# Kernel tuning notes

Measured on AMD Instinct MI355X. Metric: run time of the kernel, lower is better.

## Reference

```python
import jax, jax.numpy as jnp
import numpy as np

NN = 262144        # total nodes = 4096 graphs * 64 nodes
EN = 524288        # directed edges
IN_DIM = 32
H = 128
PROP_STEPS = 3


def setup_inputs() -> dict:
    key = jax.random.key(0)
    ks = jax.random.split(key, 16)
    s = lambda d: 1.0 / np.sqrt(d)
    x = jax.random.normal(ks[0], (NN, IN_DIM), dtype=jnp.float32)
    # edges: random within each 64-node graph block would be most faithful; random
    # over NN is the same access pattern workload-wise. Use per-graph-local edges.
    src = jax.random.randint(ks[1], (EN,), 0, NN, dtype=jnp.int64)
    dst = jax.random.randint(ks[2], (EN,), 0, NN, dtype=jnp.int64)
    edge_index = jnp.stack([src, dst], axis=0)
    return {
        "x": x,
        "edge_index": edge_index,
        "W_in": jax.random.normal(ks[3], (IN_DIM, H), jnp.float32) * s(IN_DIM),
        "b_in": jnp.zeros((H,), jnp.float32),
        "W_e1": jax.random.normal(ks[4], (H, H), jnp.float32) * s(H),
        "b_e1": jnp.zeros((H,), jnp.float32),
        "W_e2": jax.random.normal(ks[5], (H, H), jnp.float32) * s(H),
        "b_e2": jnp.zeros((H,), jnp.float32),
        "W_ih": jax.random.normal(ks[6], (H, 3 * H), jnp.float32) * s(H),
        "b_ih": jnp.zeros((3 * H,), jnp.float32),
        "W_hh": jax.random.normal(ks[7], (H, 3 * H), jnp.float32) * s(H),
        "b_hh": jnp.zeros((3 * H,), jnp.float32),
        "W_out": jax.random.normal(ks[8], (H, 1), jnp.float32) * s(H),
        "b_out": jnp.zeros((1,), jnp.float32),
    }


def reference(x, edge_index, W_in, b_in, W_e1, b_e1, W_e2, b_e2,
              W_ih, b_ih, W_hh, b_hh, W_out, b_out):
    in_node, out_node = edge_index[0], edge_index[1]
    nn = x.shape[0]
    # input MLP: Linear + tanh
    h = jnp.tanh(x @ W_in + b_in)                         # [NN, H]
    for _ in range(PROP_STEPS):
        # unified edge MLP (hidden tanh + linear out), applied per node then gathered
        m = jnp.tanh(h @ W_e1 + b_e1) @ W_e2 + b_e2       # [NN, H]
        msg = m[in_node]                                  # [EN, H] gather
        ssum = jax.ops.segment_sum(msg, out_node, num_segments=nn)
        cnt = jax.ops.segment_sum(jnp.ones((msg.shape[0],), msg.dtype),
                                  out_node, num_segments=nn)
        m_agg = ssum / jnp.maximum(cnt, 1.0)[:, None]     # scatter_mean, [NN, H]
        # GRU cell update: input = m_agg, hidden = h (torch GRUCell math)
        gi = m_agg @ W_ih + b_ih                          # [NN, 3H]
        gh = h @ W_hh + b_hh                              # [NN, 3H]
        i_r, i_z, i_n = jnp.split(gi, 3, axis=-1)
        h_r, h_z, h_n = jnp.split(gh, 3, axis=-1)
        r = jax.nn.sigmoid(i_r + h_r)
        z = jax.nn.sigmoid(i_z + h_z)
        n = jnp.tanh(i_n + r * h_n)
        h = (1.0 - z) * n + z * h
    # unified output head: single Linear
    return h @ W_out + b_out                              # [NN, 1]
```

## Files before the change

kernel.cpp:

```cpp
#include <hip/hip_runtime.h>

#define NN 262144
#define EN 524288
#define HD 128
#define IND 32

#define NT64  (NN/64)
#define GRID_E 768
#define GRID_G 1024

typedef __attribute__((ext_vector_type(8))) short s16x8;
typedef __attribute__((ext_vector_type(4))) float f32x4;
typedef unsigned short u16;
typedef unsigned int u32;

#define MFMA(a,b,c) __builtin_amdgcn_mfma_f32_16x16x32_bf16(a,b,c,0,0,0)
#define SWZ(p) ((p) ^ ((((p)>>8)&7)<<4))

typedef __attribute__((address_space(1))) void gas_void;
typedef __attribute__((address_space(3))) void las_void;
__device__ __forceinline__ void gload16(const void* g, void* l){
  __builtin_amdgcn_global_load_lds((gas_void*)g, (las_void*)l, 16, 0, 0);
}

__device__ __forceinline__ u16 f2b(float f){
  u32 u = __builtin_bit_cast(u32, f);
  u = (u + 0x7fffu + ((u >> 16) & 1u)) >> 16;
  return (u16)u;
}
__device__ __forceinline__ u32 cvtpk(float lo, float hi){
  return (u32)f2b(lo) | ((u32)f2b(hi) << 16);
}
__device__ __forceinline__ float b2f(u32 lo16){ return __builtin_bit_cast(float, lo16 << 16); }
__device__ __forceinline__ float rcpf_(float x){ return __builtin_amdgcn_rcpf(x); }
__device__ __forceinline__ float exp2_(float x){ return __builtin_amdgcn_exp2f(x); }
__device__ __forceinline__ float fsig(float x){ return rcpf_(1.f + exp2_(x * -1.442695041f)); }
__device__ __forceinline__ float ftanh(float x){ return fmaf(-2.f, rcpf_(1.f + exp2_(x * 2.885390082f)), 1.f); }

__global__ __launch_bounds__(256) void k_w2bt(const float* __restrict__ W, u16* __restrict__ Wt, int K, int N){
  int idx = blockIdx.x*256 + threadIdx.x;
  if (idx >= K*N) return;
  int n = idx / K, k = idx - n*K;
  Wt[idx] = f2b(W[k*N + n]);
}

__global__ void k_eflag(const int* __restrict__ ei, int* __restrict__ flag){
  int v = ei[threadIdx.x*2 + 1];
  unsigned long long b = __ballot(v != 0);
  if (threadIdx.x == 0) flag[0] = (b == 0ULL) ? 1 : 0;
}
__device__ __forceinline__ int eget(const int* ei, int f, int which, int e){
  return f ? ei[(which*EN + e)*2] : ei[which*EN + e];
}

__global__ __launch_bounds__(256) void k_count(const int* __restrict__ ei, const int* __restrict__ flag, int* __restrict__ cnt){
  int e = blockIdx.x*256 + threadIdx.x;
  if (e < EN) atomicAdd(&cnt[eget(ei, flag[0], 1, e)], 1);
}
__global__ __launch_bounds__(256) void k_scan1(const int* __restrict__ cnt, int* __restrict__ excl, int* __restrict__ bsum){
  __shared__ int ws[4];
  int i = blockIdx.x*256 + threadIdx.x;
  int v = cnt[i];
  int ln = threadIdx.x & 63;
  int x = v;
  #pragma unroll
  for (int d=1; d<64; d<<=1){ int y = __shfl_up(x, d); if (ln >= d) x += y; }
  if (ln == 63) ws[threadIdx.x>>6] = x;
  __syncthreads();
  int wpre = 0;
  for (int j=0; j<(threadIdx.x>>6); ++j) wpre += ws[j];
  excl[i] = wpre + x - v;
  if (threadIdx.x == 255) bsum[blockIdx.x] = wpre + x;
}
__global__ __launch_bounds__(1024) void k_scan2(int* __restrict__ bsum){
  __shared__ int ws[16];
  int i = threadIdx.x;
  int v = bsum[i];
  int ln = i & 63;
  int x = v;
  #pragma unroll
  for (int d=1; d<64; d<<=1){ int y = __shfl_up(x, d); if (ln >= d) x += y; }
  if (ln == 63) ws[i>>6] = x;
  __syncthreads();
  int wpre = 0;
  for (int j=0; j<(i>>6); ++j) wpre += ws[j];
  bsum[i] = wpre + x - v;
}
__global__ __launch_bounds__(256) void k_scan3(const int* __restrict__ excl, const int* __restrict__ bsum, int* __restrict__ rp, int* __restrict__ cur){
  int i = blockIdx.x*256 + threadIdx.x;
  int v = excl[i] + bsum[blockIdx.x];
  rp[i] = v; cur[i] = v;
  if (i == 0) rp[NN] = EN;
}
__global__ __launch_bounds__(256) void k_fill(const int* __restrict__ ei, const int* __restrict__ flag, int* __restrict__ cur, int* __restrict__ cx){
  int e = blockIdx.x*256 + threadIdx.x;
  if (e >= EN) return;
  int f = flag[0];
  int p = atomicAdd(&cur[eget(ei, f, 1, e)], 1);
  cx[p] = eget(ei, f, 0, e);
}

__global__ __launch_bounds__(256) void k_input(const float* __restrict__ x, const u16* __restrict__ wt, const float* __restrict__ bias, u16* __restrict__ h){
  const int wv = threadIdx.x >> 6, ln = threadIdx.x & 63;
  const int l15 = ln & 15, lg = ln >> 4;
  const int base = blockIdx.x*128 + wv*32;
  s16x8 a[2];
  #pragma unroll
  for (int rt=0; rt<2; ++rt){
    const float* xp = x + (base + rt*16 + l15)*IND + lg*8;
    float4 v0 = *reinterpret_cast<const float4*>(xp);
    float4 v1 = *reinterpret_cast<const float4*>(xp + 4);
    s16x8 t;
    t[0]=(short)f2b(v0.x); t[1]=(short)f2b(v0.y); t[2]=(short)f2b(v0.z); t[3]=(short)f2b(v0.w);
    t[4]=(short)f2b(v1.x); t[5]=(short)f2b(v1.y); t[6]=(short)f2b(v1.z); t[7]=(short)f2b(v1.w);
    a[rt] = t;
  }
  #pragma unroll
  for (int cg=0; cg<8; ++cg){
    const int col = cg*16 + l15;
    s16x8 bf = *reinterpret_cast<const s16x8*>(wt + col*IND + lg*8);
    float bb = bias[col];
    f32x4 acc0 = {bb,bb,bb,bb}, acc1 = {bb,bb,bb,bb};
    acc0 = MFMA(a[0], bf, acc0);
    acc1 = MFMA(a[1], bf, acc1);
    #pragma unroll
    for (int r=0; r<4; ++r){
      h[(size_t)(base + lg*4 + r)*HD + col]      = f2b(ftanh(acc0[r]));
      h[(size_t)(base + 16 + lg*4 + r)*HD + col] = f2b(ftanh(acc1[r]));
    }
  }
}

__global__ __launch_bounds__(512) void k_edge(const u16* __restrict__ h, const u16* __restrict__ wt1, const float* __restrict__ b1,
                                              const u16* __restrict__ wt2, const float* __restrict__ b2, u16* __restrict__ m){
  extern __shared__ __align__(1024) unsigned char lds[];
  const int tid = threadIdx.x, wv = tid >> 6, ln = tid & 63;
  const int l15 = ln & 15, lg = ln >> 4;
  const int col = wv*16 + l15;

  s16x8 B1[4], B2[4];
  #pragma unroll
  for (int kk=0; kk<4; ++kk){
    const int ko = kk*32 + lg*8;
    B1[kk] = *reinterpret_cast<const s16x8*>(wt1 + (size_t)col*HD + ko);
    B2[kk] = *reinterpret_cast<const s16x8*>(wt2 + (size_t)col*HD + ko);
  }
  const float b1s = b1[col], b2s = b2[col];

  {
    const unsigned char* hg = (const unsigned char*)h + (size_t)blockIdx.x*64*256;
    #pragma unroll
    for (int i=0; i<2; ++i){
      int c = wv*2 + i;
      int p = c*1024 + ln*16;
      gload16(hg + SWZ(p), lds + c*1024);
    }
  }
  __syncthreads();

  unsigned char* tl = lds + 32768;
  int t = 0;
  #pragma unroll 1
  for (int tt = blockIdx.x; tt < NT64; tt += GRID_E, ++t){
    if (tt + GRID_E < NT64){
      const unsigned char* hg = (const unsigned char*)h + (size_t)(tt+GRID_E)*64*256;
      unsigned char* dst = lds + ((t+1)&1)*16384;
      #pragma unroll
      for (int i=0; i<2; ++i){
        int c = wv*2 + i;
        int p = c*1024 + ln*16;
        gload16(hg + SWZ(p), dst + c*1024);
      }
    }
    const unsigned char* hl = lds + (t&1)*16384;
    for (int rt=0; rt<4; ++rt){
      s16x8 a[4];
      #pragma unroll
      for (int kk=0; kk<4; ++kk){
        int row = rt*16 + l15;
        int p = row*256 + (((kk*4+lg) ^ (row&7))<<4);
        a[kk] = *reinterpret_cast<const s16x8*>(hl + p);
      }
      f32x4 acc = {b1s,b1s,b1s,b1s};
      __builtin_amdgcn_s_setprio(1);
      #pragma unroll
      for (int kk=0; kk<4; ++kk) acc = MFMA(a[kk], B1[kk], acc);
      __builtin_amdgcn_s_setprio(0);
      #pragma unroll
      for (int r=0; r<4; ++r){
        int row = rt*16 + lg*4 + r;
        int tb = row*256 + ((((col*2)>>4) ^ (row&7))<<4) + ((col&7)*2);
        *reinterpret_cast<u16*>(tl + tb) = f2b(ftanh(acc[r]));
      }
    }
    __syncthreads();
    for (int rt=0; rt<4; ++rt){
      s16x8 a[4];
      #pragma unroll
      for (int kk=0; kk<4; ++kk){
        int row = rt*16 + l15;
        int p = row*256 + (((kk*4+lg) ^ (row&7))<<4);
        a[kk] = *reinterpret_cast<const s16x8*>(tl + p);
      }
      f32x4 acc = {b2s,b2s,b2s,b2s};
      __builtin_amdgcn_s_setprio(1);
      #pragma unroll
      for (int kk=0; kk<4; ++kk) acc = MFMA(a[kk], B2[kk], acc);
      __builtin_amdgcn_s_setprio(0);
      u16* mp = m + (size_t)(tt*64 + rt*16 + lg*4)*HD + col;
      mp[0]    = f2b(acc[0]);
      mp[HD]   = f2b(acc[1]);
      mp[2*HD] = f2b(acc[2]);
      mp[3*HD] = f2b(acc[3]);
    }
    __syncthreads();
  }
}

__global__ __launch_bounds__(256) void k_agg(const u16* __restrict__ m, const int* __restrict__ rp, const int* __restrict__ cx, u16* __restrict__ magg){
  const int sub = threadIdx.x >> 5, l32 = threadIdx.x & 31;
  const int n = blockIdx.x*8 + sub;
  int s0 = rp[n], s1 = rp[n+1];
  float a0=0.f, a1=0.f, a2=0.f, a3=0.f;
  int p = s0;
  for (; p + 2 <= s1; p += 2){
    int na = cx[p], nb = cx[p+1];
    uint2 va = *reinterpret_cast<const uint2*>(m + (size_t)na*HD + l32*4);
    uint2 vb = *reinterpret_cast<const uint2*>(m + (size_t)nb*HD + l32*4);
    a0 += b2f(va.x & 0xffffu) + b2f(vb.x & 0xffffu);
    a1 += b2f(va.x >> 16)     + b2f(vb.x >> 16);
    a2 += b2f(va.y & 0xffffu) + b2f(vb.y & 0xffffu);
    a3 += b2f(va.y >> 16)     + b2f(vb.y >> 16);
  }
  if (p < s1){
    int na = cx[p];
    uint2 va = *reinterpret_cast<const uint2*>(m + (size_t)na*HD + l32*4);
    a0 += b2f(va.x & 0xffffu); a1 += b2f(va.x >> 16);
    a2 += b2f(va.y & 0xffffu); a3 += b2f(va.y >> 16);
  }
  int deg = s1 - s0;
  float inv = rcpf_((float)(deg > 0 ? deg : 1));
  uint2 o;
  o.x = cvtpk(a0*inv, a1*inv);
  o.y = cvtpk(a2*inv, a3*inv);
  *reinterpret_cast<uint2*>(magg + (size_t)n*HD + l32*4) = o;
}

__global__ __launch_bounds__(256, 2) void k_gru(const u16* __restrict__ magg, const u16* __restrict__ hin, u16* __restrict__ hout,
    const u16* __restrict__ wtih, const float* __restrict__ bih,
    const u16* __restrict__ wthh, const float* __restrict__ bhh){
  extern __shared__ __align__(1024) unsigned char lds[];
  const int tid = threadIdx.x, wv = tid >> 6, ln = tid & 63;
  const int l15 = ln & 15, lg = ln >> 4;
  const int xcd = blockIdx.x & 7;
  const int q   = blockIdx.x >> 3;
  const int ch  = q & 1;
  const int p0  = (q >> 1)*8 + xcd;
  const int col = ch*64 + wv*16 + l15;
  const int ce = col & ~1;

  s16x8 B[6][4];
  #pragma unroll
  for (int kk=0; kk<4; ++kk){
    const int ko = kk*32 + lg*8;
    B[0][kk] = *reinterpret_cast<const s16x8*>(wtih + (size_t)(col       )*HD + ko);
    B[1][kk] = *reinterpret_cast<const s16x8*>(wtih + (size_t)(col +   HD)*HD + ko);
    B[2][kk] = *reinterpret_cast<const s16x8*>(wtih + (size_t)(col + 2*HD)*HD + ko);
    B[3][kk] = *reinterpret_cast<const s16x8*>(wthh + (size_t)(col       )*HD + ko);
    B[4][kk] = *reinterpret_cast<const s16x8*>(wthh + (size_t)(col +   HD)*HD + ko);
    B[5][kk] = *reinterpret_cast<const s16x8*>(wthh + (size_t)(col + 2*HD)*HD + ko);
  }
  const float brz = bih[col] + bhh[col];
  const float bzz = bih[col+HD] + bhh[col+HD];
  const float bin_ = bih[col+2*HD], bhn_ = bhh[col+2*HD];

#define LOADA(rt, amg, ahh, hld) { \
    const int row_ = (rt)*16 + l15; \
    _Pragma("unroll") \
    for (int kk=0; kk<4; ++kk){ \
      int p_ = row_*256 + (((kk*4+lg) ^ (row_&7))<<4); \
      amg[kk] = *reinterpret_cast<const s16x8*>(mgl + p_); \
      ahh[kk] = *reinterpret_cast<const s16x8*>(hl + p_); } \
    _Pragma("unroll") \
    for (int r_=0; r_<4; ++r_){ \
      int hrow_ = (rt)*16 + lg*4 + r_; \
      int hb_ = hrow_*256 + ((((ce*2)>>4) ^ (hrow_&7))<<4) + ((ce&7)*2); \
      hld[r_] = *reinterpret_cast<const u32*>(hl + hb_); } }

#define MFMAS(amg, ahh, aR, aZ, aN, aH) { \
    aR = (f32x4){brz,brz,brz,brz}; aZ = (f32x4){bzz,bzz,bzz,bzz}; \
    aN = (f32x4){bin_,bin_,bin_,bin_}; aH = (f32x4){bhn_,bhn_,bhn_,bhn_}; \
    __builtin_amdgcn_s_setprio(1); \
    _Pragma("unroll") \
    for (int kk=0; kk<4; ++kk){ \
      aR = MFMA(amg[kk], B[0][kk], aR); \
      aZ = MFMA(amg[kk], B[1][kk], aZ); \
      aN = MFMA(amg[kk], B[2][kk], aN); \
      aH = MFMA(ahh[kk], B[5][kk], aH); \
      aR = MFMA(ahh[kk], B[3][kk], aR); \
      aZ = MFMA(ahh[kk], B[4][kk], aZ); } \
    __builtin_amdgcn_s_setprio(0); }

#define EPI(rt, aR, aZ, aN, aH, hld) { \
    u16* hp_ = hout + (size_t)(rowt*64 + (rt)*16 + lg*4)*HD + col; \
    _Pragma("unroll") \
    for (int r_=0; r_<4; ++r_){ \
      float hold_ = __builtin_bit_cast(float, (col&1) ? (hld[r_] & 0xffff0000u) : (hld[r_] << 16)); \
      float rg_ = fsig(aR[r_]); \
      float zg_ = fsig(aZ[r_]); \
      float ng_ = ftanh(aN[r_] + rg_*aH[r_]); \
      hp_[r_*HD] = f2b(ng_ + zg_*(hold_ - ng_)); } }

  #pragma unroll 1
  for (int rowt = p0; rowt < NT64; rowt += 512){
    {
      const size_t rbase = (size_t)rowt*64*256;
      const unsigned char* mg = (const unsigned char*)magg + rbase;
      const unsigned char* hg = (const unsigned char*)hin  + rbase;
      #pragma unroll
      for (int i=0; i<8; ++i){
        int c = wv*8 + i;
        int p = (c & 15)*1024 + ln*16;
        gload16((c < 16 ? mg : hg) + SWZ(p), lds + c*1024);
      }
    }
    __syncthreads();

    const unsigned char* mgl = lds;
    const unsigned char* hl  = lds + 16384;

    s16x8 amgA[4], ahhA[4], amgB[4], ahhB[4];
    u32 hldA[4], hldB[4];
    f32x4 rA, zA, nA, hA, rB, zB, nB, hB;

    LOADA(0, amgA, ahhA, hldA); MFMAS(amgA, ahhA, rA, zA, nA, hA);
    LOADA(1, amgB, ahhB, hldB); MFMAS(amgB, ahhB, rB, zB, nB, hB); EPI(0, rA, zA, nA, hA, hldA);
    LOADA(2, amgA, ahhA, hldA); MFMAS(amgA, ahhA, rA, zA, nA, hA); EPI(1, rB, zB, nB, hB, hldB);
    LOADA(3, amgB, ahhB, hldB); MFMAS(amgB, ahhB, rB, zB, nB, hB); EPI(2, rA, zA, nA, hA, hldA);
    EPI(3, rB, zB, nB, hB, hldB);

    __syncthreads();
  }
#undef LOADA
#undef MFMAS
#undef EPI
}

__global__ __launch_bounds__(256) void k_out(const u16* __restrict__ h, const float* __restrict__ wo, const float* __restrict__ bo, float* __restrict__ out){
  const int wv = threadIdx.x >> 6, ln = threadIdx.x & 63;
  const int n = (blockIdx.x*4 + wv)*4 + (ln >> 4);
  const int kc = (ln & 15)*8;
  uint4 v = *reinterpret_cast<const uint4*>(h + (size_t)n*HD + kc);
  float4 w0 = *reinterpret_cast<const float4*>(wo + kc);
  float4 w1 = *reinterpret_cast<const float4*>(wo + kc + 4);
  float s = b2f(v.x & 0xffffu)*w0.x + b2f(v.x >> 16)*w0.y + b2f(v.y & 0xffffu)*w0.z + b2f(v.y >> 16)*w0.w
          + b2f(v.z & 0xffffu)*w1.x + b2f(v.z >> 16)*w1.y + b2f(v.w & 0xffffu)*w1.z + b2f(v.w >> 16)*w1.w;
  #pragma unroll
  for (int d=1; d<16; d<<=1) s += __shfl_xor(s, d, 16);
  if ((ln & 15) == 0) out[n] = s + bo[0];
}

#define AL256(x) ((((size_t)(x)) + 255) & ~(size_t)255)
static const size_t SZ_STATE = (size_t)NN*HD*2;
static const size_t OFF_HA   = 0;
static const size_t OFF_HB   = OFF_HA + SZ_STATE;
static const size_t OFF_MAGG = OFF_HB + SZ_STATE;
static const size_t OFF_RP   = OFF_MAGG + SZ_STATE;
static const size_t OFF_CUR  = OFF_RP + AL256((size_t)(NN+1)*4);
static const size_t OFF_CNT  = OFF_CUR + (size_t)NN*4;
static const size_t OFF_EXCL = OFF_CNT + (size_t)NN*4;
static const size_t OFF_BSUM = OFF_EXCL + (size_t)NN*4;
static const size_t OFF_CX   = OFF_BSUM + AL256(1024*4);
static const size_t OFF_FLAG = OFF_CX + (size_t)EN*4;
static const size_t OFF_WTIN = OFF_FLAG + 256;
static const size_t OFF_WTE1 = OFF_WTIN + AL256((size_t)IND*HD*2);
static const size_t OFF_WTE2 = OFF_WTE1 + AL256((size_t)HD*HD*2);
static const size_t OFF_WTIH = OFF_WTE2 + AL256((size_t)HD*HD*2);
static const size_t OFF_WTHH = OFF_WTIH + AL256((size_t)HD*3*HD*2);

extern "C" void kernel_launch(void* const* d_in, const int* in_sizes, int n_in,
                              void* d_out, int out_size, void* d_ws, size_t ws_size,
                              hipStream_t stream){
  const float* x    = (const float*)d_in[0];
  const int*   ei   = (const int*)d_in[1];
  const float* W_in = (const float*)d_in[2];  const float* b_in = (const float*)d_in[3];
  const float* W_e1 = (const float*)d_in[4];  const float* b_e1 = (const float*)d_in[5];
  const float* W_e2 = (const float*)d_in[6];  const float* b_e2 = (const float*)d_in[7];
  const float* W_ih = (const float*)d_in[8];  const float* b_ih = (const float*)d_in[9];
  const float* W_hh = (const float*)d_in[10]; const float* b_hh = (const float*)d_in[11];
  const float* W_out= (const float*)d_in[12]; const float* b_out= (const float*)d_in[13];
  float* out = (float*)d_out;

  char* ws = (char*)d_ws;
  u16* hA   = (u16*)(ws + OFF_HA);
  u16* hB   = (u16*)(ws + OFF_HB);
  u16* magg = (u16*)(ws + OFF_MAGG);
  int* rp   = (int*)(ws + OFF_RP);
  int* cur  = (int*)(ws + OFF_CUR);
  int* cnt  = (int*)(ws + OFF_CNT);
  int* excl = (int*)(ws + OFF_EXCL);
  int* bsum = (int*)(ws + OFF_BSUM);
  int* cx   = (int*)(ws + OFF_CX);
  int* flag = (int*)(ws + OFF_FLAG);
  u16* wtin = (u16*)(ws + OFF_WTIN);
  u16* wte1 = (u16*)(ws + OFF_WTE1);
  u16* wte2 = (u16*)(ws + OFF_WTE2);
  u16* wtih = (u16*)(ws + OFF_WTIH);
  u16* wthh = (u16*)(ws + OFF_WTHH);

  hipFuncSetAttribute((const void*)k_edge, hipFuncAttributeMaxDynamicSharedMemorySize, 49152);
  hipFuncSetAttribute((const void*)k_gru,  hipFuncAttributeMaxDynamicSharedMemorySize, 32768);

  hipMemsetAsync(cnt, 0, (size_t)NN*4, stream);

  k_w2bt<<<(IND*HD + 255)/256, 256, 0, stream>>>(W_in, wtin, IND, HD);
  k_w2bt<<<(HD*HD + 255)/256, 256, 0, stream>>>(W_e1, wte1, HD, HD);
  k_w2bt<<<(HD*HD + 255)/256, 256, 0, stream>>>(W_e2, wte2, HD, HD);
  k_w2bt<<<(HD*3*HD + 255)/256, 256, 0, stream>>>(W_ih, wtih, HD, 3*HD);
  k_w2bt<<<(HD*3*HD + 255)/256, 256, 0, stream>>>(W_hh, wthh, HD, 3*HD);

  k_eflag<<<1, 64, 0, stream>>>(ei, flag);
  k_count<<<EN/256, 256, 0, stream>>>(ei, flag, cnt);
  k_scan1<<<NN/256, 256, 0, stream>>>(cnt, excl, bsum);
  k_scan2<<<1, 1024, 0, stream>>>(bsum);
  k_scan3<<<NN/256, 256, 0, stream>>>(excl, bsum, rp, cur);
  k_fill<<<EN/256, 256, 0, stream>>>(ei, flag, cur, cx);

  k_input<<<NN/128, 256, 0, stream>>>(x, wtin, b_in, hA);

  for (int it=0; it<3; ++it){
    u16* hin  = (it & 1) ? hB : hA;
    u16* hout = (it & 1) ? hA : hB;
    k_edge<<<GRID_E, 512, 49152, stream>>>(hin, wte1, b_e1, wte2, b_e2, hout);
    k_agg<<<NN/8, 256, 0, stream>>>(hout, rp, cx, magg);
    k_gru<<<GRID_G, 256, 32768, stream>>>(magg, hin, hout, wtih, b_ih, wthh, b_hh);
  }
  k_out<<<NN/16, 256, 0, stream>>>(hB, W_out, b_out, out);
}
```

Baseline: 532.0 us.

## Split GRU kernel into input and hidden gate wave teams exchanging partials via LDS

The GRU kernel now runs 512-thread blocks in which one 4-wave team multiplies the aggregated messages by W_ih and the other multiplies the hidden state by W_hh. Each team keeps only its own weight fragments in registers, halving the per-thread weight footprint so more waves can be resident. The two teams swap partial gate sums through an extra 32 KB of LDS and take turns running the epilogue on alternate row tiles. The price is a block-wide barrier per 16-row tile, doubled LDS per block, and more LDS traffic, which may limit how many blocks fit on a CU.

```diff
diff --git a/kernel.cpp b/kernel.cpp
--- a/kernel.cpp
+++ b/kernel.cpp
@@ -7,7 +7,7 @@
 
 #define NT64  (NN/64)
 #define GRID_E 768
-#define GRID_G 1024
+#define GRID_G 512
 
 typedef __attribute__((ext_vector_type(8))) short s16x8;
 typedef __attribute__((ext_vector_type(4))) float f32x4;
@@ -246,104 +246,105 @@
   *reinterpret_cast<uint2*>(magg + (size_t)n*HD + l32*4) = o;
 }
 
-__global__ __launch_bounds__(256, 2) void k_gru(const u16* __restrict__ magg, const u16* __restrict__ hin, u16* __restrict__ hout,
+__global__ __launch_bounds__(512, 4) void k_gru(const u16* __restrict__ magg, const u16* __restrict__ hin, u16* __restrict__ hout,
     const u16* __restrict__ wtih, const float* __restrict__ bih,
     const u16* __restrict__ wthh, const float* __restrict__ bhh){
   extern __shared__ __align__(1024) unsigned char lds[];
   const int tid = threadIdx.x, wv = tid >> 6, ln = tid & 63;
   const int l15 = ln & 15, lg = ln >> 4;
+  const int team = wv >> 2;
+  const int cg   = wv & 3;
   const int xcd = blockIdx.x & 7;
   const int q   = blockIdx.x >> 3;
   const int ch  = q & 1;
-  const int p0  = (q >> 1)*8 + xcd;
-  const int col = ch*64 + wv*16 + l15;
+  const int pair = (q >> 1)*8 + xcd;
+  const int col = ch*64 + cg*16 + l15;
   const int ce = col & ~1;
 
-  s16x8 B[6][4];
+  const u16* wt = team ? wthh : wtih;
+  s16x8 B[3][4];
   #pragma unroll
   for (int kk=0; kk<4; ++kk){
     const int ko = kk*32 + lg*8;
-    B[0][kk] = *reinterpret_cast<const s16x8*>(wtih + (size_t)(col       )*HD + ko);
-    B[1][kk] = *reinterpret_cast<const s16x8*>(wtih + (size_t)(col +   HD)*HD + ko);
-    B[2][kk] = *reinterpret_cast<const s16x8*>(wtih + (size_t)(col + 2*HD)*HD + ko);
-    B[3][kk] = *reinterpret_cast<const s16x8*>(wthh + (size_t)(col       )*HD + ko);
-    B[4][kk] = *reinterpret_cast<const s16x8*>(wthh + (size_t)(col +   HD)*HD + ko);
-    B[5][kk] = *reinterpret_cast<const s16x8*>(wthh + (size_t)(col + 2*HD)*HD + ko);
+    B[0][kk] = *reinterpret_cast<const s16x8*>(wt + (size_t)(col       )*HD + ko);
+    B[1][kk] = *reinterpret_cast<const s16x8*>(wt + (size_t)(col +   HD)*HD + ko);
+    B[2][kk] = *reinterpret_cast<const s16x8*>(wt + (size_t)(col + 2*HD)*HD + ko);
   }
   const float brz = bih[col] + bhh[col];
   const float bzz = bih[col+HD] + bhh[col+HD];
   const float bin_ = bih[col+2*HD], bhn_ = bhh[col+2*HD];
-
-#define LOADA(rt, amg, ahh, hld) { \
-    const int row_ = (rt)*16 + l15; \
-    _Pragma("unroll") \
-    for (int kk=0; kk<4; ++kk){ \
-      int p_ = row_*256 + (((kk*4+lg) ^ (row_&7))<<4); \
-      amg[kk] = *reinterpret_cast<const s16x8*>(mgl + p_); \
-      ahh[kk] = *reinterpret_cast<const s16x8*>(hl + p_); } \
-    _Pragma("unroll") \
-    for (int r_=0; r_<4; ++r_){ \
-      int hrow_ = (rt)*16 + lg*4 + r_; \
-      int hb_ = hrow_*256 + ((((ce*2)>>4) ^ (hrow_&7))<<4) + ((ce&7)*2); \
-      hld[r_] = *reinterpret_cast<const u32*>(hl + hb_); } }
-
-#define MFMAS(amg, ahh, aR, aZ, aN, aH) { \
-    aR = (f32x4){brz,brz,brz,brz}; aZ = (f32x4){bzz,bzz,bzz,bzz}; \
-    aN = (f32x4){bin_,bin_,bin_,bin_}; aH = (f32x4){bhn_,bhn_,bhn_,bhn_}; \
-    __builtin_amdgcn_s_setprio(1); \
-    _Pragma("unroll") \
-    for (int kk=0; kk<4; ++kk){ \
-      aR = MFMA(amg[kk], B[0][kk], aR); \
-      aZ = MFMA(amg[kk], B[1][kk], aZ); \
-      aN = MFMA(amg[kk], B[2][kk], aN); \
-      aH = MFMA(ahh[kk], B[5][kk], aH); \
-      aR = MFMA(ahh[kk], B[3][kk], aR); \
-      aZ = MFMA(ahh[kk], B[4][kk], aZ); } \
-    __builtin_amdgcn_s_setprio(0); }
-
-#define EPI(rt, aR, aZ, aN, aH, hld) { \
-    u16* hp_ = hout + (size_t)(rowt*64 + (rt)*16 + lg*4)*HD + col; \
-    _Pragma("unroll") \
-    for (int r_=0; r_<4; ++r_){ \
-      float hold_ = __builtin_bit_cast(float, (col&1) ? (hld[r_] & 0xffff0000u) : (hld[r_] << 16)); \
-      float rg_ = fsig(aR[r_]); \
-      float zg_ = fsig(aZ[r_]); \
-      float ng_ = ftanh(aN[r_] + rg_*aH[r_]); \
-      hp_[r_*HD] = f2b(ng_ + zg_*(hold_ - ng_)); } }
+  const float i0b = team ? 0.f : brz;
+  const float i1b = team ? 0.f : bzz;
+  const float i2b = team ? bhn_ : bin_;
+
+  const unsigned char* atile = lds + team*16384;
+  const unsigned char* htile = lds + 16384;
 
   #pragma unroll 1
-  for (int rowt = p0; rowt < NT64; rowt += 512){
+  for (int rowt = pair; rowt < NT64; rowt += 256){
     {
       const size_t rbase = (size_t)rowt*64*256;
       const unsigned char* mg = (const unsigned char*)magg + rbase;
       const unsigned char* hg = (const unsigned char*)hin  + rbase;
       #pragma unroll
-      for (int i=0; i<8; ++i){
-        int c = wv*8 + i;
+      for (int i=0; i<4; ++i){
+        int c = wv*4 + i;
         int p = (c & 15)*1024 + ln*16;
         gload16((c < 16 ? mg : hg) + SWZ(p), lds + c*1024);
       }
     }
     __syncthreads();
 
-    const unsigned char* mgl = lds;
-    const unsigned char* hl  = lds + 16384;
-
-    s16x8 amgA[4], ahhA[4], amgB[4], ahhB[4];
-    u32 hldA[4], hldB[4];
-    f32x4 rA, zA, nA, hA, rB, zB, nB, hB;
-
-    LOADA(0, amgA, ahhA, hldA); MFMAS(amgA, ahhA, rA, zA, nA, hA);
-    LOADA(1, amgB, ahhB, hldB); MFMAS(amgB, ahhB, rB, zB, nB, hB); EPI(0, rA, zA, nA, hA, hldA);
-    LOADA(2, amgA, ahhA, hldA); MFMAS(amgA, ahhA, rA, zA, nA, hA); EPI(1, rB, zB, nB, hB, hldB);
-    LOADA(3, amgB, ahhB, hldB); MFMAS(amgB, ahhB, rB, zB, nB, hB); EPI(2, rA, zA, nA, hA, hldA);
-    EPI(3, rB, zB, nB, hB, hldB);
-
+    #pragma unroll
+    for (int rt=0; rt<4; ++rt){
+      s16x8 a[4];
+      #pragma unroll
+      for (int kk=0; kk<4; ++kk){
+        int row = rt*16 + l15;
+        int p = row*256 + (((kk*4+lg) ^ (row&7))<<4);
+        a[kk] = *reinterpret_cast<const s16x8*>(atile + p);
+      }
+      f32x4 acc0 = {i0b,i0b,i0b,i0b}, acc1 = {i1b,i1b,i1b,i1b}, acc2 = {i2b,i2b,i2b,i2b};
+      __builtin_amdgcn_s_setprio(1);
+      #pragma unroll
+      for (int kk=0; kk<4; ++kk){
+        acc0 = MFMA(a[kk], B[0][kk], acc0);
+        acc1 = MFMA(a[kk], B[1][kk], acc1);
+        acc2 = MFMA(a[kk], B[2][kk], acc2);
+      }
+      __builtin_amdgcn_s_setprio(0);
+
+      float* xb = (float*)(lds + 32768) + (rt&1)*4096 + (cg*64 + ln)*16;
+      const int ep = rt & 1;
+      if (team != ep){
+        *reinterpret_cast<f32x4*>(xb)     = acc0;
+        *reinterpret_cast<f32x4*>(xb + 4) = acc1;
+        *reinterpret_cast<f32x4*>(xb + 8) = acc2;
+      }
+      __syncthreads();
+      if (team == ep){
+        f32x4 p0 = *reinterpret_cast<const f32x4*>(xb);
+        f32x4 p1 = *reinterpret_cast<const f32x4*>(xb + 4);
+        f32x4 p2 = *reinterpret_cast<const f32x4*>(xb + 8);
+        f32x4 i0, i1, i2, h0, h1, h2;
+        if ((rt & 1) == 0){ i0=acc0; i1=acc1; i2=acc2; h0=p0; h1=p1; h2=p2; }
+        else              { i0=p0; i1=p1; i2=p2; h0=acc0; h1=acc1; h2=acc2; }
+        u16* hp = hout + (size_t)(rowt*64 + rt*16 + lg*4)*HD + col;
+        #pragma unroll
+        for (int r=0; r<4; ++r){
+          int hrow = rt*16 + lg*4 + r;
+          int hb = hrow*256 + ((((ce*2)>>4) ^ (hrow&7))<<4) + ((ce&7)*2);
+          u32 pr = *reinterpret_cast<const u32*>(htile + hb);
+          float hold = __builtin_bit_cast(float, (col&1) ? (pr & 0xffff0000u) : (pr << 16));
+          float rg = fsig(i0[r] + h0[r]);
+          float zg = fsig(i1[r] + h1[r]);
+          float ng = ftanh(i2[r] + rg*h2[r]);
+          hp[r*HD] = f2b(ng + zg*(hold - ng));
+        }
+      }
+    }
     __syncthreads();
   }
-#undef LOADA
-#undef MFMAS
-#undef EPI
 }
 
 __global__ __launch_bounds__(256) void k_out(const u16* __restrict__ h, const float* __restrict__ wo, const float* __restrict__ bo, float* __restrict__ out){
@@ -409,7 +410,7 @@
   u16* wthh = (u16*)(ws + OFF_WTHH);
 
   hipFuncSetAttribute((const void*)k_edge, hipFuncAttributeMaxDynamicSharedMemorySize, 49152);
-  hipFuncSetAttribute((const void*)k_gru,  hipFuncAttributeMaxDynamicSharedMemorySize, 32768);
+  hipFuncSetAttribute((const void*)k_gru,  hipFuncAttributeMaxDynamicSharedMemorySize, 65536);
 
   hipMemsetAsync(cnt, 0, (size_t)NN*4, stream);
 
@@ -433,7 +434,7 @@
     u16* hout = (it & 1) ? hA : hB;
     k_edge<<<GRID_E, 512, 49152, stream>>>(hin, wte1, b_e1, wte2, b_e2, hout);
     k_agg<<<NN/8, 256, 0, stream>>>(hout, rp, cx, magg);
-    k_gru<<<GRID_G, 256, 32768, stream>>>(magg, hin, hout, wtih, b_ih, wthh, b_hh);
+    k_gru<<<GRID_G, 512, 65536, stream>>>(magg, hin, hout, wtih, b_ih, wthh, b_hh);
   }
   k_out<<<NN/16, 256, 0, stream>>>(hB, W_out, b_out, out);
 }
```

After: 589.7 us. +10.8%, slower.
